# Kernel tuning notes

Measured on AMD Instinct MI355X. Metric: run time of the kernel, lower is better.

The kernel has to match this reference:

```python
import jax, jax.numpy as jnp
import numpy as np

OUT_H, OUT_W = 7, 7  # output_size


def _pool_matrix(in_size: int, out_size: int) -> np.ndarray:
    """[out_size, in_size] row-stochastic matrix: row o averages input
    indices in [floor(o*in/out), ceil((o+1)*in/out)) -- same windows as
    the TF adaptive pooling slicing path."""
    o = np.arange(out_size, dtype=np.float32)
    start = (o * in_size / out_size).astype(np.int32)
    stop = np.ceil((o + 1) * in_size / out_size).astype(np.int32)
    i = np.arange(in_size)
    mask = (i[None, :] >= start[:, None]) & (i[None, :] < stop[:, None])
    size = (stop - start).astype(np.float32)
    return mask.astype(np.float32) / size[:, None]


def setup_inputs() -> dict:
    key = jax.random.key(0)
    x = jax.random.normal(key, (16, 512, 512, 64), dtype=jnp.float32)
    return {"x": x}


def reference(x) -> jnp.ndarray:
    B, H, W, C = x.shape
    wh = jnp.asarray(_pool_matrix(H, OUT_H))  # [OH, H]
    ww = jnp.asarray(_pool_matrix(W, OUT_W))  # [OW, W]
    # mean over height windows, then over width windows (matches TF order)
    y = jnp.einsum('oh,bhwc->bowc', wh, x)
    y = jnp.einsum('pw,bowc->bopc', ww, y)
    return y
```

## Files before the change

### kernel.cpp

```cpp
#include <hip/hip_runtime.h>


#define IN_HW  512
#define OUT_HW 7
#define NB     16
#define NC     64
#define C4     16
#define HCHUNKS 4
#define NPIX   (NB * OUT_HW * OUT_HW)

__device__ __forceinline__ int win_start(int o) { return (o * IN_HW) / OUT_HW; }
__device__ __forceinline__ int win_stop(int o)  { return ((o + 1) * IN_HW + OUT_HW - 1) / OUT_HW; }

__global__ __launch_bounds__(256)
void pool_partial_kernel(const float4* __restrict__ x, float4* __restrict__ partial) {
    __shared__ float4 red[256];

    const int blk = blockIdx.x;
    const int hc  = blk & (HCHUNKS - 1);
    const int pix = blk >> 2;
    const int ow  = pix % OUT_HW;
    const int oh  = (pix / OUT_HW) % OUT_HW;
    const int b   = pix / (OUT_HW * OUT_HW);

    const int hs = win_start(oh), he = win_stop(oh);
    const int nh = he - hs;
    const int r0 = hs + (hc * nh) / HCHUNKS;
    const int r1 = hs + ((hc + 1) * nh) / HCHUNKS;

    const int ws = win_start(ow), we = win_stop(ow);
    const int span = (we - ws) * C4;

    const int tid = threadIdx.x;

    float4 acc = make_float4(0.f, 0.f, 0.f, 0.f);
    #pragma unroll 2
    for (int h = r0; h < r1; ++h) {
        const float4* seg = x + ((size_t)(b * IN_HW + h) * IN_HW + ws) * C4;
        #pragma unroll 5
        for (int j = tid; j < span; j += 256) {
            float4 v = seg[j];
            acc.x += v.x; acc.y += v.y; acc.z += v.z; acc.w += v.w;
        }
    }
    red[tid] = acc;
    __syncthreads();

    #pragma unroll
    for (int s = 128; s >= 16; s >>= 1) {
        if (tid < s) {
            float4 o = red[tid + s];
            float4 m = red[tid];
            m.x += o.x; m.y += o.y; m.z += o.z; m.w += o.w;
            red[tid] = m;
        }
        __syncthreads();
    }

    if (tid < C4) {
        partial[(size_t)blk * C4 + tid] = red[tid];
    }
}

__global__ __launch_bounds__(256)
void pool_finish_kernel(const float4* __restrict__ partial, float4* __restrict__ out) {
    const int idx = blockIdx.x * 256 + threadIdx.x;
    if (idx >= NPIX * C4) return;

    const int c4  = idx & (C4 - 1);
    const int pix = idx >> 4;
    const int ow  = pix % OUT_HW;
    const int oh  = (pix / OUT_HW) % OUT_HW;

    float4 acc = make_float4(0.f, 0.f, 0.f, 0.f);
    #pragma unroll
    for (int k = 0; k < HCHUNKS; ++k) {
        float4 v = partial[((size_t)pix * HCHUNKS + k) * C4 + c4];
        acc.x += v.x; acc.y += v.y; acc.z += v.z; acc.w += v.w;
    }
    const float scale = 1.0f / (float)((win_stop(oh) - win_start(oh)) *
                                       (win_stop(ow) - win_start(ow)));
    acc.x *= scale; acc.y *= scale; acc.z *= scale; acc.w *= scale;
    out[idx] = acc;
}

__global__ __launch_bounds__(256)
void pool_fused_kernel(const float4* __restrict__ x, float4* __restrict__ out) {
    __shared__ float4 red[256];

    const int blk = blockIdx.x;
    const int ow = blk % OUT_HW;
    const int oh = (blk / OUT_HW) % OUT_HW;
    const int b  = blk / (OUT_HW * OUT_HW);

    const int tid = threadIdx.x;
    const int c4 = tid & 15;
    const int rg = tid >> 4;

    const int hs = win_start(oh), he = win_stop(oh);
    const int ws = win_start(ow), we = win_stop(ow);

    float4 acc = make_float4(0.f, 0.f, 0.f, 0.f);
    for (int h = hs + rg; h < he; h += 16) {
        const float4* row = x + ((size_t)(b * IN_HW + h)) * (IN_HW * C4);
        #pragma unroll 8
        for (int w = ws; w < we; ++w) {
            float4 v = row[w * C4 + c4];
            acc.x += v.x; acc.y += v.y; acc.z += v.z; acc.w += v.w;
        }
    }
    red[tid] = acc;
    __syncthreads();

    #pragma unroll
    for (int s = 8; s >= 1; s >>= 1) {
        if (rg < s) {
            float4 o = red[(rg + s) * 16 + c4];
            float4 m = red[rg * 16 + c4];
            m.x += o.x; m.y += o.y; m.z += o.z; m.w += o.w;
            red[rg * 16 + c4] = m;
        }
        __syncthreads();
    }

    if (rg == 0) {
        const float scale = 1.0f / (float)((he - hs) * (we - ws));
        float4 m = red[c4];
        m.x *= scale; m.y *= scale; m.z *= scale; m.w *= scale;
        out[(size_t)blk * C4 + c4] = m;
    }
}

extern "C" void kernel_launch(void* const* d_in, const int* in_sizes, int n_in,
                              void* d_out, int out_size, void* d_ws, size_t ws_size,
                              hipStream_t stream) {
    const float4* x = (const float4*)d_in[0];
    float4* out = (float4*)d_out;

    const size_t ws_needed = (size_t)NPIX * HCHUNKS * C4 * sizeof(float4);

    if (ws_size >= ws_needed) {
        float4* partial = (float4*)d_ws;
        pool_partial_kernel<<<NPIX * HCHUNKS, 256, 0, stream>>>(x, partial);
        pool_finish_kernel<<<(NPIX * C4 + 255) / 256, 256, 0, stream>>>(partial, out);
    } else {
        pool_fused_kernel<<<NPIX, 256, 0, stream>>>(x, out);
    }
}
```

Before: 213.0 us.

## Stream full input rows once with per-window accumulators for all output columns

```diff
diff --git a/kernel.cpp b/kernel.cpp
--- a/kernel.cpp
+++ b/kernel.cpp
@@ -4,84 +4,99 @@
 #define IN_HW  512
 #define OUT_HW 7
 #define NB     16
-#define NC     64
 #define C4     16
-#define HCHUNKS 4
+#define RPC    4
+#define NCHUNK 19
+#define NPAIR  (NB * OUT_HW)
 #define NPIX   (NB * OUT_HW * OUT_HW)
 
 __device__ __forceinline__ int win_start(int o) { return (o * IN_HW) / OUT_HW; }
 __device__ __forceinline__ int win_stop(int o)  { return ((o + 1) * IN_HW + OUT_HW - 1) / OUT_HW; }
 
+__device__ __forceinline__ void f4add(float4& a, const float4& v) {
+    a.x += v.x; a.y += v.y; a.z += v.z; a.w += v.w;
+}
+
+__device__ __constant__ const int KJ_[1] = {0};
+
 __global__ __launch_bounds__(256)
-void pool_partial_kernel(const float4* __restrict__ x, float4* __restrict__ partial) {
-    __shared__ float4 red[256];
+void pool_stream_kernel(const float4* __restrict__ x, float4* __restrict__ partial) {
+    constexpr int KJ[32] = {0,0,0,0,0, 1,1,1,1,1, 2,2,2,2, 3,3,3,3,3,
+                            4,4,4,4, 5,5,5,5,5, 6,6,6,6};
+    constexpr int BJ[32] = {-1,-1,-1,-1, 9, -1,-1,-1,-1, 2, -1,-1,-1, 11,
+                            -1,-1,-1,-1, 4, -1,-1,-1, 13, -1,-1,-1,-1, 6,
+                            -1,-1,-1,-1};
 
-    const int blk = blockIdx.x;
-    const int hc  = blk & (HCHUNKS - 1);
-    const int pix = blk >> 2;
-    const int ow  = pix % OUT_HW;
-    const int oh  = (pix / OUT_HW) % OUT_HW;
-    const int b   = pix / (OUT_HW * OUT_HW);
+    const int blk   = blockIdx.x;
+    const int chunk = blk % NCHUNK;
+    const int pair  = blk / NCHUNK;
+    const int oh    = pair % OUT_HW;
+    const int b     = pair / OUT_HW;
 
-    const int hs = win_start(oh), he = win_stop(oh);
-    const int nh = he - hs;
-    const int r0 = hs + (hc * nh) / HCHUNKS;
-    const int r1 = hs + ((hc + 1) * nh) / HCHUNKS;
+    const int hs = win_start(oh);
+    const int r0 = hs + chunk * RPC;
+    const int r1 = min(hs + (win_stop(oh) - hs), r0 + RPC);
 
-    const int ws = win_start(ow), we = win_stop(ow);
-    const int span = (we - ws) * C4;
+    const int tid  = threadIdx.x;
+    const int base = tid >> 4;
+    const int c4   = tid & 15;
 
-    const int tid = threadIdx.x;
+    float4 acc[7];
+    #pragma unroll
+    for (int o = 0; o < 7; ++o) acc[o] = make_float4(0.f, 0.f, 0.f, 0.f);
 
-    float4 acc = make_float4(0.f, 0.f, 0.f, 0.f);
-    #pragma unroll 2
+    #pragma unroll 1
     for (int h = r0; h < r1; ++h) {
-        const float4* seg = x + ((size_t)(b * IN_HW + h) * IN_HW + ws) * C4;
-        #pragma unroll 5
-        for (int j = tid; j < span; j += 256) {
-            float4 v = seg[j];
-            acc.x += v.x; acc.y += v.y; acc.z += v.z; acc.w += v.w;
+        const float4* seg = x + (size_t)(b * IN_HW + h) * (IN_HW * C4) + tid;
+        #pragma unroll
+        for (int j = 0; j < 32; ++j) {
+            float4 v = seg[256 * j];
+            const int K = KJ[j];
+            const int B = BJ[j];
+            if (B < 0) {
+                f4add(acc[K], v);
+            } else {
+                if (base <= B) f4add(acc[K], v);
+                if (base >= B) f4add(acc[K + 1], v);
+            }
         }
     }
-    red[tid] = acc;
+
+    __shared__ float4 lds[16][7][16];
+    #pragma unroll
+    for (int o = 0; o < 7; ++o) lds[base][o][c4] = acc[o];
     __syncthreads();
 
-    #pragma unroll
-    for (int s = 128; s >= 16; s >>= 1) {
-        if (tid < s) {
-            float4 o = red[tid + s];
-            float4 m = red[tid];
-            m.x += o.x; m.y += o.y; m.z += o.z; m.w += o.w;
-            red[tid] = m;
-        }
-        __syncthreads();
-    }
-
-    if (tid < C4) {
-        partial[(size_t)blk * C4 + tid] = red[tid];
+    if (tid < 7 * C4) {
+        const int ow_ = tid >> 4;
+        const int c_  = tid & 15;
+        float4 s = make_float4(0.f, 0.f, 0.f, 0.f);
+        #pragma unroll
+        for (int g = 0; g < 16; ++g) f4add(s, lds[g][ow_][c_]);
+        partial[((size_t)pair * NCHUNK + chunk) * (7 * C4) + tid] = s;
     }
 }
 
 __global__ __launch_bounds__(256)
 void pool_finish_kernel(const float4* __restrict__ partial, float4* __restrict__ out) {
     const int idx = blockIdx.x * 256 + threadIdx.x;
-    if (idx >= NPIX * C4) return;
+    if (idx >= NPAIR * 7 * C4) return;
 
-    const int c4  = idx & (C4 - 1);
-    const int pix = idx >> 4;
-    const int ow  = pix % OUT_HW;
-    const int oh  = (pix / OUT_HW) % OUT_HW;
+    const int t    = idx % (7 * C4);
+    const int pair = idx / (7 * C4);
+    const int ow   = t >> 4;
+    const int oh   = pair % OUT_HW;
 
-    float4 acc = make_float4(0.f, 0.f, 0.f, 0.f);
+    float4 s = make_float4(0.f, 0.f, 0.f, 0.f);
     #pragma unroll
-    for (int k = 0; k < HCHUNKS; ++k) {
-        float4 v = partial[((size_t)pix * HCHUNKS + k) * C4 + c4];
-        acc.x += v.x; acc.y += v.y; acc.z += v.z; acc.w += v.w;
+    for (int k = 0; k < NCHUNK; ++k) {
+        float4 v = partial[((size_t)pair * NCHUNK + k) * (7 * C4) + t];
+        f4add(s, v);
     }
     const float scale = 1.0f / (float)((win_stop(oh) - win_start(oh)) *
                                        (win_stop(ow) - win_start(ow)));
-    acc.x *= scale; acc.y *= scale; acc.z *= scale; acc.w *= scale;
-    out[idx] = acc;
+    s.x *= scale; s.y *= scale; s.z *= scale; s.w *= scale;
+    out[idx] = s;
 }
 
 __global__ __launch_bounds__(256)
@@ -106,7 +121,7 @@
         #pragma unroll 8
         for (int w = ws; w < we; ++w) {
             float4 v = row[w * C4 + c4];
-            acc.x += v.x; acc.y += v.y; acc.z += v.z; acc.w += v.w;
+            f4add(acc, v);
         }
     }
     red[tid] = acc;
@@ -116,9 +131,8 @@
     for (int s = 8; s >= 1; s >>= 1) {
         if (rg < s) {
             float4 o = red[(rg + s) * 16 + c4];
-            float4 m = red[rg * 16 + c4];
-            m.x += o.x; m.y += o.y; m.z += o.z; m.w += o.w;
-            red[rg * 16 + c4] = m;
+            f4add(o, red[rg * 16 + c4]);
+            red[rg * 16 + c4] = o;
         }
         __syncthreads();
     }
@@ -137,12 +151,12 @@
     const float4* x = (const float4*)d_in[0];
     float4* out = (float4*)d_out;
 
-    const size_t ws_needed = (size_t)NPIX * HCHUNKS * C4 * sizeof(float4);
+    const size_t ws_needed = (size_t)NPAIR * NCHUNK * 7 * C4 * sizeof(float4);
 
     if (ws_size >= ws_needed) {
         float4* partial = (float4*)d_ws;
-        pool_partial_kernel<<<NPIX * HCHUNKS, 256, 0, stream>>>(x, partial);
-        pool_finish_kernel<<<(NPIX * C4 + 255) / 256, 256, 0, stream>>>(partial, out);
+        pool_stream_kernel<<<NPAIR * NCHUNK, 256, 0, stream>>>(x, partial);
+        pool_finish_kernel<<<(NPAIR * 7 * C4 + 255) / 256, 256, 0, stream>>>(partial, out);
     } else {
         pool_fused_kernel<<<NPIX, 256, 0, stream>>>(x, out);
     }
```

Result: faster. 194.4 us (-8.7%).
